# Performance work log

Measured on AMD Instinct MI355X. Metric: run time of the kernel, lower is better.

## Reference

```python
import jax, jax.numpy as jnp
import numpy as np

N = 100000      # nodes
E = 1600000     # graph edges (avg degree 16)
Q = 1000000     # query edges to score
IN, HID, OUT = 128, 128, 64


def setup_inputs() -> dict:
    key = jax.random.key(0)
    ks = jax.random.split(key, 7)
    feat = jax.random.normal(ks[0], (N, IN), dtype=jnp.float32)
    edge_src = jax.random.randint(ks[1], (E,), 0, N, dtype=jnp.int32)
    edge_dst = jax.random.randint(ks[2], (E,), 0, N, dtype=jnp.int32)
    src = jax.random.randint(ks[3], (Q,), 0, N, dtype=jnp.int32)
    dst = jax.random.randint(ks[4], (Q,), 0, N, dtype=jnp.int32)
    W1 = jax.random.normal(ks[5], (IN, HID), dtype=jnp.float32) / np.sqrt(IN).astype(np.float32)
    b1 = jnp.zeros((HID,), jnp.float32)
    W2 = jax.random.normal(ks[6], (HID, OUT), dtype=jnp.float32) / np.sqrt(HID).astype(np.float32)
    b2 = jnp.zeros((OUT,), jnp.float32)
    return {"feat": feat, "edge_src": edge_src, "edge_dst": edge_dst,
            "src": src, "dst": dst, "W1": W1, "b1": b1, "W2": W2, "b2": b2}


def _graph_conv(h, W, b, edge_src, edge_dst, out_norm, in_norm):
    """DGL GraphConv(norm='both'): D_out^{-1/2} -> aggregate -> D_in^{-1/2}, W, b.
    DGL applies W before aggregation when in_feats > out_feats (same math)."""
    n = h.shape[0]
    h = h * out_norm[:, None]
    if h.shape[1] > W.shape[1]:
        h = h @ W
        agg = jax.ops.segment_sum(h[edge_src], edge_dst, num_segments=n)
    else:
        agg = jax.ops.segment_sum(h[edge_src], edge_dst, num_segments=n)
        agg = agg @ W
    return agg * in_norm[:, None] + b


def reference(feat, edge_src, edge_dst, src, dst, W1, b1, W2, b2):
    n = feat.shape[0]
    ones = jnp.ones((edge_src.shape[0],), feat.dtype)
    out_deg = jax.ops.segment_sum(ones, edge_src, num_segments=n)
    in_deg = jax.ops.segment_sum(ones, edge_dst, num_segments=n)
    out_norm = jnp.maximum(out_deg, 1.0) ** -0.5
    in_norm = jnp.maximum(in_deg, 1.0) ** -0.5

    h = _graph_conv(feat, W1, b1, edge_src, edge_dst, out_norm, in_norm)
    h = jax.nn.relu(h)  # dropout is identity at inference
    h = _graph_conv(h, W2, b2, edge_src, edge_dst, out_norm, in_norm)

    edge_scores = jnp.sum(h[src] * h[dst], axis=-1)
    return jax.nn.sigmoid(edge_scores)
```

## Files before the change

kernel.cpp:

```cpp
#include <hip/hip_runtime.h>
#include <math.h>

static inline size_t align256(size_t x) { return (x + 255) & ~(size_t)255; }

typedef __attribute__((ext_vector_type(8))) short bf16x8;
typedef __attribute__((ext_vector_type(4))) float f32x4;

__device__ inline float bfLo(unsigned int u) {
  union { unsigned int i; float f; } v; v.i = u << 16; return v.f;
}
__device__ inline float bfHi(unsigned int u) {
  union { unsigned int i; float f; } v; v.i = u & 0xffff0000u; return v.f;
}
__device__ inline float bf2f(unsigned short u) {
  union { unsigned int i; float f; } v; v.i = ((unsigned int)u) << 16; return v.f;
}
__device__ inline unsigned short f2bf(float f) {
  union { float f; unsigned int i; } v; v.f = f;
  unsigned int r = v.i + 0x7FFF + ((v.i >> 16) & 1);
  return (unsigned short)(r >> 16);
}
__device__ inline unsigned int packbf(float lo, float hi) {
  return ((unsigned int)f2bf(hi) << 16) | f2bf(lo);
}

__global__ __launch_bounds__(256) void k_coarse_count(const int* __restrict__ esrc,
                                                      const int* __restrict__ edst,
                                                      int E, int chunk, int NB, int G,
                                                      int* __restrict__ blkD,
                                                      int* __restrict__ blkS) {
  __shared__ int hD[512], hS[512];
  int blk = blockIdx.x, tid = threadIdx.x;
  for (int i = tid; i < NB; i += 256) { hD[i] = 0; hS[i] = 0; }
  __syncthreads();
  int s0 = blk * chunk, s1 = min(E, s0 + chunk);
  for (int e = s0 + tid; e < s1; e += 256) {
    atomicAdd(&hD[edst[e] >> 8], 1);
    atomicAdd(&hS[esrc[e] >> 8], 1);
  }
  __syncthreads();
  for (int i = tid; i < NB; i += 256) {
    blkD[i * G + blk] = hD[i];
    blkS[i * G + blk] = hS[i];
  }
}

__global__ __launch_bounds__(256) void k_scan1(const int* __restrict__ in,
                                               int* __restrict__ out,
                                               int* __restrict__ bsums, int n) {
  __shared__ int s[256];
  int tid = threadIdx.x, gid = blockIdx.x * 256 + tid;
  int v = (gid < n) ? in[gid] : 0;
  s[tid] = v; __syncthreads();
  for (int o = 1; o < 256; o <<= 1) {
    int t = (tid >= o) ? s[tid - o] : 0;
    __syncthreads();
    s[tid] += t;
    __syncthreads();
  }
  if (gid < n) out[gid] = s[tid] - v;
  if (tid == 255) bsums[blockIdx.x] = s[255];
}

__global__ __launch_bounds__(512) void k_scan2(int* __restrict__ bsums, int nb) {
  __shared__ int s[512];
  int tid = threadIdx.x;
  int* base = bsums + blockIdx.x * nb;
  int v = (tid < nb) ? base[tid] : 0;
  s[tid] = v; __syncthreads();
  for (int o = 1; o < 512; o <<= 1) {
    int t = (tid >= o) ? s[tid - o] : 0;
    __syncthreads();
    s[tid] += t;
    __syncthreads();
  }
  if (tid < nb) base[tid] = s[tid] - v;
}

__global__ __launch_bounds__(256) void k_scan3b(int* __restrict__ arr,
                                                const int* __restrict__ bsums, int n) {
  int gid = blockIdx.x * 256 + threadIdx.x;
  if (gid < n) arr[gid] += bsums[blockIdx.x];
}

__global__ __launch_bounds__(256) void k_coarse_scatter(const int* __restrict__ esrc,
                                                        const int* __restrict__ edst,
                                                        int E, int chunk, int NB, int G,
                                                        const int* __restrict__ scD,
                                                        const int* __restrict__ scS,
                                                        unsigned int* __restrict__ pairs,
                                                        unsigned int* __restrict__ keys) {
  __shared__ int cD[512], cS[512];
  int blk = blockIdx.x, tid = threadIdx.x;
  for (int i = tid; i < NB; i += 256) {
    cD[i] = scD[i * G + blk];
    cS[i] = scS[i * G + blk];
  }
  __syncthreads();
  int s0 = blk * chunk, s1 = min(E, s0 + chunk);
  for (int e = s0 + tid; e < s1; e += 256) {
    int s = esrc[e], d = edst[e];
    int pd = atomicAdd(&cD[d >> 8], 1);
    pairs[pd] = ((unsigned)s << 8) | ((unsigned)d & 255u);
    int ps = atomicAdd(&cS[s >> 8], 1);
    keys[ps] = (unsigned)s;
  }
}

__global__ __launch_bounds__(256) void k_fine(const unsigned int* __restrict__ pairs,
                                              const unsigned int* __restrict__ keys,
                                              const int* __restrict__ scD,
                                              const int* __restrict__ scS,
                                              int G, int E, int N, int NB,
                                              int* __restrict__ cntIn,
                                              float* __restrict__ normIn,
                                              int* __restrict__ offs,
                                              int* __restrict__ csr,
                                              float* __restrict__ normOut) {
  __shared__ int hist[256], scn[256], cur[256];
  int tid = threadIdx.x;
  if (blockIdx.x >= (unsigned)NB) {
    int b = blockIdx.x - NB;
    int bstart = scS[b * G];
    int bend = (b + 1 < NB) ? scS[(b + 1) * G] : E;
    hist[tid] = 0;
    __syncthreads();
    for (int e = bstart + tid; e < bend; e += 256)
      atomicAdd(&hist[keys[e] & 255u], 1);
    __syncthreads();
    int node = b * 256 + tid;
    if (node < N) normOut[node] = rsqrtf((float)max(hist[tid], 1));
    return;
  }
  int b = blockIdx.x;
  int bstart = scD[b * G];
  int bend = (b + 1 < NB) ? scD[(b + 1) * G] : E;
  hist[tid] = 0;
  __syncthreads();
  for (int e = bstart + tid; e < bend; e += 256)
    atomicAdd(&hist[pairs[e] & 255u], 1);
  __syncthreads();
  int v = hist[tid];
  scn[tid] = v;
  __syncthreads();
  for (int o = 1; o < 256; o <<= 1) {
    int t = (tid >= o) ? scn[tid - o] : 0;
    __syncthreads();
    scn[tid] += t;
    __syncthreads();
  }
  int excl = scn[tid] - v;
  cur[tid] = excl;
  int node = b * 256 + tid;
  if (node < N) {
    cntIn[node] = v;
    normIn[node] = rsqrtf((float)max(v, 1));
    offs[node] = bstart + excl;
  }
  __syncthreads();
  for (int e = bstart + tid; e < bend; e += 256) {
    unsigned int u = pairs[e];
    int p = bstart + atomicAdd(&cur[u & 255u], 1);
    csr[p] = (int)(u >> 8);
  }
}

__global__ __launch_bounds__(256) void k_prep(const float* __restrict__ W1,
                                              const float* __restrict__ W2,
                                              unsigned short* __restrict__ W1t,
                                              unsigned short* __restrict__ W2t) {
  int t = blockIdx.x * 256 + threadIdx.x;
  int stride = gridDim.x * 256;
  for (int i = t; i < 128 * 128; i += stride) {
    int nn = i >> 7, kk = i & 127;
    W1t[i] = f2bf(W1[kk * 128 + nn]);
  }
  for (int i = t; i < 64 * 128; i += stride) {
    int nn = i >> 7, kk = i & 127;
    W2t[i] = f2bf(W2[kk * 64 + nn]);
  }
}

template <int C, typename TA>
__global__ __launch_bounds__(256) void k_mgemm(const TA* __restrict__ A,
                                               const float* __restrict__ scale,
                                               const unsigned short* __restrict__ Wt,
                                               unsigned short* __restrict__ out, int n) {
  constexpr int KP = 136;
  constexpr int NCH = C / 16;
  __shared__ __align__(16) unsigned short Al[64 * KP];
  __shared__ __align__(16) unsigned short Wl[C * KP];
  int tid = threadIdx.x;
  int r0 = blockIdx.x * 64;

  {
    const uint4* Wg = (const uint4*)Wt;
    uint4* Wd = (uint4*)Wl;
    for (int idx = tid; idx < C * 16; idx += 256) {
      int row = idx >> 4, seg = idx & 15;
      Wd[row * 17 + seg] = Wg[idx];
    }
  }
  {
    int seg = tid & 7;
    for (int it = 0; it < 2; ++it) {
      int row = (tid >> 3) + it * 32;
      int g = r0 + row;
      float v[16];
      if (g < n) {
        float sc = scale[g];
        if constexpr (sizeof(TA) == 4) {
          const float4* Ag = (const float4*)((const float*)A + (size_t)g * 128);
#pragma unroll
          for (int j = 0; j < 4; ++j) {
            float4 f = Ag[seg * 4 + j];
            v[j * 4 + 0] = f.x * sc; v[j * 4 + 1] = f.y * sc;
            v[j * 4 + 2] = f.z * sc; v[j * 4 + 3] = f.w * sc;
          }
        } else {
          const uint4* Ag = (const uint4*)((const unsigned short*)A + (size_t)g * 128);
#pragma unroll
          for (int j = 0; j < 2; ++j) {
            uint4 u = Ag[seg * 2 + j];
            v[j * 8 + 0] = bfLo(u.x) * sc; v[j * 8 + 1] = bfHi(u.x) * sc;
            v[j * 8 + 2] = bfLo(u.y) * sc; v[j * 8 + 3] = bfHi(u.y) * sc;
            v[j * 8 + 4] = bfLo(u.z) * sc; v[j * 8 + 5] = bfHi(u.z) * sc;
            v[j * 8 + 6] = bfLo(u.w) * sc; v[j * 8 + 7] = bfHi(u.w) * sc;
          }
        }
      } else {
#pragma unroll
        for (int j = 0; j < 16; ++j) v[j] = 0.f;
      }
      uint4* dst = (uint4*)(Al + row * KP + seg * 16);
      dst[0] = make_uint4(packbf(v[0], v[1]), packbf(v[2], v[3]),
                          packbf(v[4], v[5]), packbf(v[6], v[7]));
      dst[1] = make_uint4(packbf(v[8], v[9]), packbf(v[10], v[11]),
                          packbf(v[12], v[13]), packbf(v[14], v[15]));
    }
  }
  __syncthreads();

  int lane = tid & 63;
  int w = tid >> 6;
  int quad = lane >> 4, m16 = lane & 15;
  f32x4 acc[NCH];
#pragma unroll
  for (int c = 0; c < NCH; ++c) acc[c] = (f32x4){0.f, 0.f, 0.f, 0.f};

#pragma unroll
  for (int kc = 0; kc < 4; ++kc) {
    int ko = kc * 32 + quad * 8;
    bf16x8 a = *(const bf16x8*)(Al + (w * 16 + m16) * KP + ko);
#pragma unroll
    for (int c = 0; c < NCH; ++c) {
      bf16x8 b = *(const bf16x8*)(Wl + (c * 16 + m16) * KP + ko);
      acc[c] = __builtin_amdgcn_mfma_f32_16x16x32_bf16(a, b, acc[c], 0, 0, 0);
    }
  }

#pragma unroll
  for (int c = 0; c < NCH; ++c)
#pragma unroll
    for (int r = 0; r < 4; ++r) {
      int g = r0 + w * 16 + quad * 4 + r;
      if (g < n) out[(size_t)g * C + c * 16 + m16] = f2bf(acc[c][r]);
    }
}

__global__ __launch_bounds__(256) void k_agg128_relu(const unsigned short* __restrict__ X,
                                                     const int* __restrict__ csr,
                                                     const int* __restrict__ offs,
                                                     const int* __restrict__ cnt,
                                                     const float* __restrict__ norm,
                                                     const float* __restrict__ bias,
                                                     unsigned short* __restrict__ H, int n) {
  int wid = blockIdx.x * 4 + (threadIdx.x >> 6);
  if (wid >= n) return;
  int lane = threadIdx.x & 63;
  int start = offs[wid], m = cnt[wid];
  const int* p = csr + start;
  const unsigned int* Xu = (const unsigned int*)X;
  float ax = 0.f, ay = 0.f;
  for (int c0 = 0; c0 < m; c0 += 64) {
    int take = min(64, m - c0);
    int iv = p[c0 + ((lane < take) ? lane : take - 1)];
    int e = 0;
    for (; e + 16 <= take; e += 16) {
      int ss[16]; unsigned int uu[16];
#pragma unroll
      for (int j = 0; j < 16; ++j) ss[j] = __shfl(iv, e + j);
#pragma unroll
      for (int j = 0; j < 16; ++j) uu[j] = Xu[(size_t)ss[j] * 64 + lane];
#pragma unroll
      for (int j = 0; j < 16; ++j) { ax += bfLo(uu[j]); ay += bfHi(uu[j]); }
    }
    for (; e + 4 <= take; e += 4) {
      int ss[4]; unsigned int uu[4];
#pragma unroll
      for (int j = 0; j < 4; ++j) ss[j] = __shfl(iv, e + j);
#pragma unroll
      for (int j = 0; j < 4; ++j) uu[j] = Xu[(size_t)ss[j] * 64 + lane];
#pragma unroll
      for (int j = 0; j < 4; ++j) { ax += bfLo(uu[j]); ay += bfHi(uu[j]); }
    }
    for (; e < take; ++e) {
      unsigned int u = Xu[(size_t)__shfl(iv, e) * 64 + lane];
      ax += bfLo(u); ay += bfHi(u);
    }
  }
  float nm = norm[wid];
  float2 b = ((const float2*)bias)[lane];
  float ox = fmaxf(ax * nm + b.x, 0.f);
  float oy = fmaxf(ay * nm + b.y, 0.f);
  ((unsigned int*)H)[(size_t)wid * 64 + lane] = packbf(ox, oy);
}

__global__ __launch_bounds__(256) void k_agg64(const unsigned short* __restrict__ X,
                                               const int* __restrict__ csr,
                                               const int* __restrict__ offs,
                                               const int* __restrict__ cnt,
                                               const float* __restrict__ norm,
                                               const float* __restrict__ bias,
                                               unsigned short* __restrict__ H, int n) {
  int wid = blockIdx.x * 4 + (threadIdx.x >> 6);
  if (wid >= n) return;
  int lane = threadIdx.x & 63;
  int start = offs[wid], m = cnt[wid];
  const int* p = csr + start;
  float a = 0.f;
  for (int c0 = 0; c0 < m; c0 += 64) {
    int take = min(64, m - c0);
    int iv = p[c0 + ((lane < take) ? lane : take - 1)];
    int e = 0;
    for (; e + 16 <= take; e += 16) {
      int ss[16]; unsigned short uu[16];
#pragma unroll
      for (int j = 0; j < 16; ++j) ss[j] = __shfl(iv, e + j);
#pragma unroll
      for (int j = 0; j < 16; ++j) uu[j] = X[(size_t)ss[j] * 64 + lane];
#pragma unroll
      for (int j = 0; j < 16; ++j) a += bf2f(uu[j]);
    }
    for (; e + 4 <= take; e += 4) {
      int ss[4]; unsigned short uu[4];
#pragma unroll
      for (int j = 0; j < 4; ++j) ss[j] = __shfl(iv, e + j);
#pragma unroll
      for (int j = 0; j < 4; ++j) uu[j] = X[(size_t)ss[j] * 64 + lane];
#pragma unroll
      for (int j = 0; j < 4; ++j) a += bf2f(uu[j]);
    }
    for (; e < take; ++e) a += bf2f(X[(size_t)__shfl(iv, e) * 64 + lane]);
  }
  H[(size_t)wid * 64 + lane] = f2bf(a * norm[wid] + bias[lane]);
}

__global__ __launch_bounds__(256) void k_score(const unsigned short* __restrict__ H,
                                               const int* __restrict__ qs,
                                               const int* __restrict__ qd,
                                               float* __restrict__ out, int q) {
  int t = blockIdx.x * 256 + threadIdx.x;
  int sub = t & 15;
  int q0 = t >> 4;
  float p = 0.f;
  if (q0 < q) {
    int s = qs[q0], d = qd[q0];
    const uint2* Hu = (const uint2*)H;
    uint2 a = Hu[(size_t)s * 16 + sub];
    uint2 b = Hu[(size_t)d * 16 + sub];
    p = bfLo(a.x) * bfLo(b.x) + bfHi(a.x) * bfHi(b.x) +
        bfLo(a.y) * bfLo(b.y) + bfHi(a.y) * bfHi(b.y);
  }
  p += __shfl_xor(p, 1);
  p += __shfl_xor(p, 2);
  p += __shfl_xor(p, 4);
  p += __shfl_xor(p, 8);
  if (sub == 0 && q0 < q) out[q0] = 1.f / (1.f + expf(-p));
}

extern "C" void kernel_launch(void* const* d_in, const int* in_sizes, int n_in,
                              void* d_out, int out_size, void* d_ws, size_t ws_size,
                              hipStream_t stream) {
  const float* feat = (const float*)d_in[0];
  const int* esrc   = (const int*)d_in[1];
  const int* edst   = (const int*)d_in[2];
  const int* qsrc   = (const int*)d_in[3];
  const int* qdst   = (const int*)d_in[4];
  const float* W1   = (const float*)d_in[5];
  const float* b1   = (const float*)d_in[6];
  const float* W2   = (const float*)d_in[7];
  const float* b2   = (const float*)d_in[8];
  float* out = (float*)d_out;

  const int N = in_sizes[0] / 128;
  const int E = in_sizes[1];
  const int Q = in_sizes[3];

  const int G = 256;
  const int NB = (N + 255) >> 8;
  const int chunk = (E + G - 1) / G;
  const int lenS = NB * G;
  const int gScan = lenS / 256;

  char* w = (char*)d_ws;
  size_t o = 0;
  unsigned short* X1 = (unsigned short*)(w + o); o += align256((size_t)N * 128 * 2);
  unsigned short* X2 = (unsigned short*)(w + o); o += align256((size_t)N * 64 * 2);
  unsigned short* H2 = (unsigned short*)(w + o); o += align256((size_t)N * 64 * 2);
  int* cntIn = (int*)(w + o);       o += align256((size_t)N * 4);
  float* normOut = (float*)(w + o); o += align256((size_t)N * 4);
  float* normIn = (float*)(w + o);  o += align256((size_t)N * 4);
  int* offs = (int*)(w + o);        o += align256((size_t)N * 4);
  int* blk = (int*)(w + o);         o += align256((size_t)lenS * 8);
  int* sc = (int*)(w + o);          o += align256((size_t)lenS * 8);
  int* bsums = (int*)(w + o);       o += align256((size_t)8192);
  unsigned short* W1t = (unsigned short*)(w + o); o += align256((size_t)128 * 128 * 2);
  unsigned short* W2t = (unsigned short*)(w + o); o += align256((size_t)64 * 128 * 2);
  unsigned int* pairs = (unsigned int*)(w + o); o += align256((size_t)E * 4);
  unsigned int* keys = (unsigned int*)(w + o); o += align256((size_t)E * 4);
  int* csr = (int*)(w + o);         o += align256((size_t)E * 4);

  int* blkD = blk;        int* blkS = blk + lenS;
  int* scD = sc;          int* scS = sc + lenS;

  k_prep<<<64, 256, 0, stream>>>(W1, W2, W1t, W2t);

  k_coarse_count<<<G, 256, 0, stream>>>(esrc, edst, E, chunk, NB, G, blkD, blkS);
  k_scan1<<<2 * gScan, 256, 0, stream>>>(blk, sc, bsums, 2 * lenS);
  k_scan2<<<2, 512, 0, stream>>>(bsums, gScan);
  k_scan3b<<<2 * gScan, 256, 0, stream>>>(sc, bsums, 2 * lenS);
  k_coarse_scatter<<<G, 256, 0, stream>>>(esrc, edst, E, chunk, NB, G, scD, scS, pairs, keys);
  k_fine<<<2 * NB, 256, 0, stream>>>(pairs, keys, scD, scS, G, E, N, NB,
                                     cntIn, normIn, offs, csr, normOut);

  const int gRows = (N + 63) / 64;
  k_mgemm<128, float><<<gRows, 256, 0, stream>>>(feat, normOut, W1t, X1, N);
  k_agg128_relu<<<(N + 3) / 4, 256, 0, stream>>>(X1, csr, offs, cntIn, normIn, b1, X2, N);
  k_mgemm<64, unsigned short><<<gRows, 256, 0, stream>>>(X2, normOut, W2t, X1, N);
  k_agg64<<<(N + 3) / 4, 256, 0, stream>>>(X1, csr, offs, cntIn, normIn, b2, H2, N);
  k_score<<<((Q * 16) + 255) / 256, 256, 0, stream>>>(H2, qsrc, qdst, out, Q);
}
```

Baseline: 355.1 us.

## Use 16-byte vector gathers with multiple edges per wavefront in aggregation and scoring

The two aggregation kernels now split each wavefront into lane groups, each loading one whole neighbor row slice as a uint4. Several edges are processed at once, and cross-group shuffles reduce the partial sums. The scoring kernel uses 8 lanes per query with uint4 loads instead of 16 lanes with uint2. The aim is fewer, wider memory requests and better lane use for low-degree nodes. The cost is more registers and extra shuffle reductions at the end.

```diff
diff --git a/kernel.cpp b/kernel.cpp
--- a/kernel.cpp
+++ b/kernel.cpp
@@ -278,42 +278,72 @@
   int wid = blockIdx.x * 4 + (threadIdx.x >> 6);
   if (wid >= n) return;
   int lane = threadIdx.x & 63;
+  int sub = lane & 15;
+  int grp = lane >> 4;
   int start = offs[wid], m = cnt[wid];
   const int* p = csr + start;
-  const unsigned int* Xu = (const unsigned int*)X;
-  float ax = 0.f, ay = 0.f;
+  const uint4* Xv = (const uint4*)X;
+  float a[8] = {0.f, 0.f, 0.f, 0.f, 0.f, 0.f, 0.f, 0.f};
   for (int c0 = 0; c0 < m; c0 += 64) {
     int take = min(64, m - c0);
     int iv = p[c0 + ((lane < take) ? lane : take - 1)];
     int e = 0;
     for (; e + 16 <= take; e += 16) {
-      int ss[16]; unsigned int uu[16];
-#pragma unroll
-      for (int j = 0; j < 16; ++j) ss[j] = __shfl(iv, e + j);
-#pragma unroll
-      for (int j = 0; j < 16; ++j) uu[j] = Xu[(size_t)ss[j] * 64 + lane];
-#pragma unroll
-      for (int j = 0; j < 16; ++j) { ax += bfLo(uu[j]); ay += bfHi(uu[j]); }
+      uint4 uu[4];
+#pragma unroll
+      for (int j = 0; j < 4; ++j) {
+        int ss = __shfl(iv, e + j * 4 + grp);
+        uu[j] = Xv[(size_t)ss * 16 + sub];
+      }
+#pragma unroll
+      for (int j = 0; j < 4; ++j) {
+        a[0] += bfLo(uu[j].x); a[1] += bfHi(uu[j].x);
+        a[2] += bfLo(uu[j].y); a[3] += bfHi(uu[j].y);
+        a[4] += bfLo(uu[j].z); a[5] += bfHi(uu[j].z);
+        a[6] += bfLo(uu[j].w); a[7] += bfHi(uu[j].w);
+      }
     }
     for (; e + 4 <= take; e += 4) {
-      int ss[4]; unsigned int uu[4];
-#pragma unroll
-      for (int j = 0; j < 4; ++j) ss[j] = __shfl(iv, e + j);
-#pragma unroll
-      for (int j = 0; j < 4; ++j) uu[j] = Xu[(size_t)ss[j] * 64 + lane];
-#pragma unroll
-      for (int j = 0; j < 4; ++j) { ax += bfLo(uu[j]); ay += bfHi(uu[j]); }
-    }
-    for (; e < take; ++e) {
-      unsigned int u = Xu[(size_t)__shfl(iv, e) * 64 + lane];
-      ax += bfLo(u); ay += bfHi(u);
-    }
+      int ss = __shfl(iv, e + grp);
+      uint4 u = Xv[(size_t)ss * 16 + sub];
+      a[0] += bfLo(u.x); a[1] += bfHi(u.x);
+      a[2] += bfLo(u.y); a[3] += bfHi(u.y);
+      a[4] += bfLo(u.z); a[5] += bfHi(u.z);
+      a[6] += bfLo(u.w); a[7] += bfHi(u.w);
+    }
+    int r = take - e;
+    if (r > 0) {
+      int ss = __shfl(iv, min(e + grp, take - 1));
+      uint4 u = Xv[(size_t)ss * 16 + sub];
+      if (grp < r) {
+        a[0] += bfLo(u.x); a[1] += bfHi(u.x);
+        a[2] += bfLo(u.y); a[3] += bfHi(u.y);
+        a[4] += bfLo(u.z); a[5] += bfHi(u.z);
+        a[6] += bfLo(u.w); a[7] += bfHi(u.w);
+      }
+    }
+  }
+#pragma unroll
+  for (int k = 0; k < 8; ++k) {
+    a[k] += __shfl_xor(a[k], 16);
+    a[k] += __shfl_xor(a[k], 32);
   }
   float nm = norm[wid];
-  float2 b = ((const float2*)bias)[lane];
-  float ox = fmaxf(ax * nm + b.x, 0.f);
-  float oy = fmaxf(ay * nm + b.y, 0.f);
-  ((unsigned int*)H)[(size_t)wid * 64 + lane] = packbf(ox, oy);
+  const float4* bv = (const float4*)bias;
+  float4 b0 = bv[sub * 2], b1 = bv[sub * 2 + 1];
+  if (grp == 0) {
+    float o0 = fmaxf(a[0] * nm + b0.x, 0.f);
+    float o1 = fmaxf(a[1] * nm + b0.y, 0.f);
+    float o2 = fmaxf(a[2] * nm + b0.z, 0.f);
+    float o3 = fmaxf(a[3] * nm + b0.w, 0.f);
+    float o4 = fmaxf(a[4] * nm + b1.x, 0.f);
+    float o5 = fmaxf(a[5] * nm + b1.y, 0.f);
+    float o6 = fmaxf(a[6] * nm + b1.z, 0.f);
+    float o7 = fmaxf(a[7] * nm + b1.w, 0.f);
+    uint4 o = make_uint4(packbf(o0, o1), packbf(o2, o3),
+                         packbf(o4, o5), packbf(o6, o7));
+    ((uint4*)H)[(size_t)wid * 16 + sub] = o;
+  }
 }
 
 __global__ __launch_bounds__(256) void k_agg64(const unsigned short* __restrict__ X,
@@ -326,34 +356,67 @@
   int wid = blockIdx.x * 4 + (threadIdx.x >> 6);
   if (wid >= n) return;
   int lane = threadIdx.x & 63;
+  int sub = lane & 7;
+  int grp = lane >> 3;
   int start = offs[wid], m = cnt[wid];
   const int* p = csr + start;
-  float a = 0.f;
+  const uint4* Xv = (const uint4*)X;
+  float a[8] = {0.f, 0.f, 0.f, 0.f, 0.f, 0.f, 0.f, 0.f};
   for (int c0 = 0; c0 < m; c0 += 64) {
     int take = min(64, m - c0);
     int iv = p[c0 + ((lane < take) ? lane : take - 1)];
     int e = 0;
     for (; e + 16 <= take; e += 16) {
-      int ss[16]; unsigned short uu[16];
-#pragma unroll
-      for (int j = 0; j < 16; ++j) ss[j] = __shfl(iv, e + j);
-#pragma unroll
-      for (int j = 0; j < 16; ++j) uu[j] = X[(size_t)ss[j] * 64 + lane];
-#pragma unroll
-      for (int j = 0; j < 16; ++j) a += bf2f(uu[j]);
-    }
-    for (; e + 4 <= take; e += 4) {
-      int ss[4]; unsigned short uu[4];
-#pragma unroll
-      for (int j = 0; j < 4; ++j) ss[j] = __shfl(iv, e + j);
-#pragma unroll
-      for (int j = 0; j < 4; ++j) uu[j] = X[(size_t)ss[j] * 64 + lane];
-#pragma unroll
-      for (int j = 0; j < 4; ++j) a += bf2f(uu[j]);
-    }
-    for (; e < take; ++e) a += bf2f(X[(size_t)__shfl(iv, e) * 64 + lane]);
-  }
-  H[(size_t)wid * 64 + lane] = f2bf(a * norm[wid] + bias[lane]);
+      uint4 uu[2];
+#pragma unroll
+      for (int j = 0; j < 2; ++j) {
+        int ss = __shfl(iv, e + j * 8 + grp);
+        uu[j] = Xv[(size_t)ss * 8 + sub];
+      }
+#pragma unroll
+      for (int j = 0; j < 2; ++j) {
+        a[0] += bfLo(uu[j].x); a[1] += bfHi(uu[j].x);
+        a[2] += bfLo(uu[j].y); a[3] += bfHi(uu[j].y);
+        a[4] += bfLo(uu[j].z); a[5] += bfHi(uu[j].z);
+        a[6] += bfLo(uu[j].w); a[7] += bfHi(uu[j].w);
+      }
+    }
+    for (; e + 8 <= take; e += 8) {
+      int ss = __shfl(iv, e + grp);
+      uint4 u = Xv[(size_t)ss * 8 + sub];
+      a[0] += bfLo(u.x); a[1] += bfHi(u.x);
+      a[2] += bfLo(u.y); a[3] += bfHi(u.y);
+      a[4] += bfLo(u.z); a[5] += bfHi(u.z);
+      a[6] += bfLo(u.w); a[7] += bfHi(u.w);
+    }
+    int r = take - e;
+    if (r > 0) {
+      int ss = __shfl(iv, min(e + grp, take - 1));
+      uint4 u = Xv[(size_t)ss * 8 + sub];
+      if (grp < r) {
+        a[0] += bfLo(u.x); a[1] += bfHi(u.x);
+        a[2] += bfLo(u.y); a[3] += bfHi(u.y);
+        a[4] += bfLo(u.z); a[5] += bfHi(u.z);
+        a[6] += bfLo(u.w); a[7] += bfHi(u.w);
+      }
+    }
+  }
+#pragma unroll
+  for (int k = 0; k < 8; ++k) {
+    a[k] += __shfl_xor(a[k], 8);
+    a[k] += __shfl_xor(a[k], 16);
+    a[k] += __shfl_xor(a[k], 32);
+  }
+  float nm = norm[wid];
+  const float4* bv = (const float4*)bias;
+  float4 b0 = bv[sub * 2], b1 = bv[sub * 2 + 1];
+  if (grp == 0) {
+    uint4 o = make_uint4(packbf(a[0] * nm + b0.x, a[1] * nm + b0.y),
+                         packbf(a[2] * nm + b0.z, a[3] * nm + b0.w),
+                         packbf(a[4] * nm + b1.x, a[5] * nm + b1.y),
+                         packbf(a[6] * nm + b1.z, a[7] * nm + b1.w));
+    ((uint4*)H)[(size_t)wid * 8 + sub] = o;
+  }
 }
 
 __global__ __launch_bounds__(256) void k_score(const unsigned short* __restrict__ H,
@@ -361,21 +424,22 @@
                                                const int* __restrict__ qd,
                                                float* __restrict__ out, int q) {
   int t = blockIdx.x * 256 + threadIdx.x;
-  int sub = t & 15;
-  int q0 = t >> 4;
+  int sub = t & 7;
+  int q0 = t >> 3;
   float p = 0.f;
   if (q0 < q) {
     int s = qs[q0], d = qd[q0];
-    const uint2* Hu = (const uint2*)H;
-    uint2 a = Hu[(size_t)s * 16 + sub];
-    uint2 b = Hu[(size_t)d * 16 + sub];
+    const uint4* Hv = (const uint4*)H;
+    uint4 a = Hv[(size_t)s * 8 + sub];
+    uint4 b = Hv[(size_t)d * 8 + sub];
     p = bfLo(a.x) * bfLo(b.x) + bfHi(a.x) * bfHi(b.x) +
-        bfLo(a.y) * bfLo(b.y) + bfHi(a.y) * bfHi(b.y);
+        bfLo(a.y) * bfLo(b.y) + bfHi(a.y) * bfHi(b.y) +
+        bfLo(a.z) * bfLo(b.z) + bfHi(a.z) * bfHi(b.z) +
+        bfLo(a.w) * bfLo(b.w) + bfHi(a.w) * bfHi(b.w);
   }
   p += __shfl_xor(p, 1);
   p += __shfl_xor(p, 2);
   p += __shfl_xor(p, 4);
-  p += __shfl_xor(p, 8);
   if (sub == 0 && q0 < q) out[q0] = 1.f / (1.f + expf(-p));
 }
 
@@ -439,5 +503,5 @@
   k_agg128_relu<<<(N + 3) / 4, 256, 0, stream>>>(X1, csr, offs, cntIn, normIn, b1, X2, N);
   k_mgemm<64, unsigned short><<<gRows, 256, 0, stream>>>(X2, normOut, W2t, X1, N);
   k_agg64<<<(N + 3) / 4, 256, 0, stream>>>(X1, csr, offs, cntIn, normIn, b2, H2, N);
-  k_score<<<((Q * 16) + 255) / 256, 256, 0, stream>>>(H2, qsrc, qdst, out, Q);
-}
+  k_score<<<((Q * 8) + 255) / 256, 256, 0, stream>>>(H2, qsrc, qdst, out, Q);
+}
```

Measured after the change: 325.3 us. -8.4%, faster.
